# Optimization experiments

Measured on AMD Instinct MI355X. Metric: run time of the kernel, lower is better.

Reference implementation:

```python
import jax, jax.numpy as jnp
import numpy as np

LAYERS = 20
STACKS = 2
LPS = LAYERS // STACKS  # layers per stack -> dilations 2**(l % LPS)
OUT_CH = 256
RES_CH = 64
GATE_CH = 128
SKIP_CH = 256


def setup_inputs() -> dict:
    key = jax.random.key(0)
    ks = jax.random.split(key, 16)
    B, T = 8, 16000
    s = 0.05
    inp = {
        "x": jax.random.normal(ks[0], (B, OUT_CH, T), dtype=jnp.float32),
        # first causal conv (note: original code applies w_pre to the shifted
        # input twice -> output is 2*w_pre(pre); w_cur is unused, so omitted)
        "w_pre0": jax.random.normal(ks[1], (RES_CH, OUT_CH)) * s,
        "b_pre0": jax.random.normal(ks[2], (RES_CH,)) * s,
        # per-layer dilated conv (no bias), residual block, skip projection
        "w_dil_pre": jax.random.normal(ks[3], (LAYERS, GATE_CH, RES_CH)) * s,
        "w_dil_cur": jax.random.normal(ks[4], (LAYERS, GATE_CH, RES_CH)) * s,
        "bias_h": jax.random.normal(ks[5], (LAYERS, GATE_CH)) * s,
        "w_res": jax.random.normal(ks[6], (LAYERS, RES_CH, RES_CH)) * s,
        "b_res": jax.random.normal(ks[7], (LAYERS, RES_CH)) * s,
        "w_skip": jax.random.normal(ks[8], (LAYERS, SKIP_CH, RES_CH)) * s,
        "b_skip": jax.random.normal(ks[9], (LAYERS, SKIP_CH)) * s,
        # output head
        "w_relu": jax.random.normal(ks[10], (SKIP_CH, SKIP_CH)) * s,
        "b_relu": jax.random.normal(ks[11], (SKIP_CH,)) * s,
        "w_out": jax.random.normal(ks[12], (OUT_CH, SKIP_CH)) * s,
        "b_out": jax.random.normal(ks[13], (OUT_CH,)) * s,
    }
    return inp


def _shift_right(h, d):
    # causal shift: pad d zeros on the left along time, drop last d samples
    return jnp.pad(h, ((0, 0), (0, 0), (d, 0)))[:, :, :-d]


def reference(x, w_pre0, b_pre0, w_dil_pre, w_dil_cur, bias_h,
              w_res, b_res, w_skip, b_skip, w_relu, b_relu, w_out, b_out):
    # first causal conv: original Conv2X1 'casual' path computes
    # w_pre(pre) + w_pre(pre) = 2 * w_pre(pre)  (faithful to source)
    pre = _shift_right(x, 1)
    h = 2.0 * (jnp.einsum('rc,bct->brt', w_pre0, pre) + b_pre0[None, :, None])

    skip = jnp.zeros((x.shape[0], SKIP_CH, x.shape[2]), dtype=h.dtype)
    for l in range(LAYERS):
        d = 2 ** (l % LPS)
        h_pre = _shift_right(h, d)
        # dilated 2x1 conv = two channel-wise linears (no bias), summed with bias_h
        a = (jnp.einsum('gr,brt->bgt', w_dil_pre[l], h_pre)
             + jnp.einsum('gr,brt->bgt', w_dil_cur[l], h)
             + bias_h[l][None, :, None])
        g = jnp.tanh(a[:, :RES_CH]) * jax.nn.sigmoid(a[:, RES_CH:])
        res = jnp.einsum('rq,bqt->brt', w_res[l], g) + b_res[l][None, :, None]
        h = h + res
        skip = skip + jnp.einsum('sr,brt->bst', w_skip[l], g) + b_skip[l][None, :, None]

    o = jax.nn.relu(skip)
    o = jnp.einsum('ps,bst->bpt', w_relu, o) + b_relu[None, :, None]
    o = jax.nn.relu(o)
    logits = jnp.einsum('os,bst->bot', w_out, o) + b_out[None, :, None]
    return jax.nn.softmax(logits, axis=1)  # (B, out_channels, T)
```

## Files before the change

### kernel.cpp

```cpp
#include <hip/hip_runtime.h>
#include <math.h>

#define B_ 8
#define T_ 16000
#define NBT 250
#define HROWS 16512
#define NLAY 20

typedef __attribute__((ext_vector_type(8))) short bf16x8;
typedef __attribute__((ext_vector_type(4))) float f32x4;
typedef __attribute__((ext_vector_type(4))) short sh4;

__device__ __forceinline__ unsigned short f2bf(float f){
  unsigned u = __float_as_uint(f);
  u += 0x7fffu + ((u >> 16) & 1u);
  return (unsigned short)(u >> 16);
}
__device__ __forceinline__ float bf2f(unsigned short s){
  return __uint_as_float(((unsigned)s) << 16);
}
__device__ __forceinline__ void split2(float v, unsigned short& hi, unsigned short& lo){
  hi = f2bf(v);
  lo = f2bf(v - bf2f(hi));
}

#define MFMA(a,b,c) __builtin_amdgcn_mfma_f32_16x16x32_bf16((a),(b),(c),0,0,0)

__device__ __forceinline__ void gload16(const short* gsrc, short* ldst){
  __builtin_amdgcn_global_load_lds(
      (const __attribute__((address_space(1))) unsigned int*)gsrc,
      (__attribute__((address_space(3))) unsigned int*)ldst, 16, 0, 0);
}

__global__ void k_split(const float* __restrict__ src, short* __restrict__ hi,
                        short* __restrict__ lo, int n){
  int idx = blockIdx.x * 256 + threadIdx.x;
  if (idx < n){
    unsigned short h, l; split2(src[idx], h, l);
    hi[idx] = (short)h; lo[idx] = (short)l;
  }
}
__global__ void k_split_gate(const float* __restrict__ wdp, const float* __restrict__ wdc,
                             short* __restrict__ hi, short* __restrict__ lo){
  int idx = blockIdx.x * 256 + threadIdx.x;
  if (idx < NLAY*128*128){
    int l   = idx >> 14;
    int rem = idx & 16383;
    int row = rem >> 7;
    int k   = rem & 127;
    float v = (k < 64) ? wdp[(l*128 + row)*64 + k] : wdc[(l*128 + row)*64 + (k-64)];
    unsigned short h, lo16; split2(v, h, lo16);
    hi[idx] = (short)h; lo[idx] = (short)lo16;
  }
}
__global__ void k_pack_wsf(const float* __restrict__ wsk, short* __restrict__ wsf){
  int idx = blockIdx.x * 256 + threadIdx.x;
  if (idx < NLAY*8*2*2*64*8){
    int e    = idx & 7;
    int j    = (idx >> 3) & 63;
    int kb2  = (idx >> 9) & 1;
    int half = (idx >> 10) & 1;
    int w    = (idx >> 11) & 7;
    int l    = idx >> 14;
    int row  = w*32 + half*16 + (j & 15);
    int ch   = (kb2*4 + (j >> 4))*8 + e;
    wsf[idx] = (short)f2bf(wsk[((size_t)l*256 + row)*64 + ch]);
  }
}
__global__ void k_bsum(const float* __restrict__ bsk, float* __restrict__ bsum){
  int s = threadIdx.x;
  if (s < 256){
    float a = 0.f;
#pragma unroll
    for (int l = 0; l < NLAY; ++l) a += bsk[l*256 + s];
    bsum[s] = a;
  }
}
__global__ void k_zero_guard(short* __restrict__ hA, short* __restrict__ hB){
  int idx = blockIdx.x * 256 + threadIdx.x;
  if (idx < B_*512*128){
    int b = idx / (512*128);
    int rem = idx - b*(512*128);
    size_t off = (size_t)b*HROWS*128 + rem;
    hA[off] = 0; hB[off] = 0;
  }
}

__global__ __launch_bounds__(512) void k_head_in(
    const float* __restrict__ x, const short* __restrict__ wph,
    const short* __restrict__ wpl, const float* __restrict__ bias,
    short* __restrict__ h)
{
  __shared__ short SXh[64*256], SXl[64*256];
  const int tid = threadIdx.x;
  const int bb = blockIdx.x / NBT;
  const int t0 = (blockIdx.x % NBT) * 64;
  const int lane = tid & 63, w = tid >> 6;
  const int l16 = lane & 15, l4 = lane >> 4;

  const float* xb = x + (size_t)bb * 256 * T_;
  {
    int col = lane;
    int t = t0 + col - 1;
#pragma unroll
    for (int p = 0; p < 16; ++p){
      int k0 = w*32 + p*2;
      float v0 = (t >= 0) ? xb[(size_t)k0*T_ + t] : 0.f;
      float v1 = (t >= 0) ? xb[(size_t)(k0+1)*T_ + t] : 0.f;
      unsigned short h0,l0,h1,l1; split2(v0,h0,l0); split2(v1,h1,l1);
      int idx = col*256 + (k0 ^ ((col & 15) << 3));
      ((unsigned int*)SXh)[idx>>1] = (unsigned)h0 | ((unsigned)h1 << 16);
      ((unsigned int*)SXl)[idx>>1] = (unsigned)l0 | ((unsigned)l1 << 16);
    }
  }
  __syncthreads();

  const int mi = w & 3, nh = w >> 2;
  const int rowA = mi*16 + l16;
  const int rt0 = mi*16 + l4*4;
  bf16x8 Ah[8], Al[8];
#pragma unroll
  for (int kb = 0; kb < 8; ++kb){
    int ko = kb*32 + l4*8;
    Ah[kb] = *(const bf16x8*)(wph + (size_t)rowA*256 + ko);
    Al[kb] = *(const bf16x8*)(wpl + (size_t)rowA*256 + ko);
  }
  short* hb = h + ((size_t)bb*HROWS + 512)*128;
#pragma unroll
  for (int nt = 0; nt < 2; ++nt){
    int col = (nh*2 + nt)*16 + l16;
    f32x4 acc = {0.f,0.f,0.f,0.f};
#pragma unroll
    for (int kb = 0; kb < 8; ++kb){
      int ko = (kb*32 + l4*8) ^ (l16 << 3);
      bf16x8 bhv = *(const bf16x8*)&SXh[col*256 + ko];
      bf16x8 blv = *(const bf16x8*)&SXl[col*256 + ko];
      acc = MFMA(Ah[kb], bhv, acc);
      acc = MFMA(Ah[kb], blv, acc);
      acc = MFMA(Al[kb], bhv, acc);
    }
    int t = t0 + col;
    int key = t & 15;
    int c  = rt0 >> 3, sub = rt0 & 7;
    sh4 hv, lv;
#pragma unroll
    for (int r = 0; r < 4; ++r){
      float v = 2.f*(acc[r] + bias[rt0 + r]);
      unsigned short hh, ll; split2(v, hh, ll);
      hv[r] = (short)hh; lv[r] = (short)ll;
    }
    *(sh4*)&hb[(size_t)t*128 + ((c ^ key) << 3) + sub] = hv;
    *(sh4*)&hb[(size_t)t*128 + (((c + 8) ^ key) << 3) + sub] = lv;
  }
}

__global__ __launch_bounds__(512, 6) void k_layer6(
    const short* __restrict__ hin, short* __restrict__ hout,
    short* __restrict__ gout,
    const short* __restrict__ wgh, const short* __restrict__ wgl,
    const short* __restrict__ wrh, const short* __restrict__ wrlo,
    const float* __restrict__ bh, const float* __restrict__ br, int d)
{
  __shared__ short SH[64*128];
  __shared__ short SHP[64*128];
  const int tid = threadIdx.x;
  const int bb = blockIdx.x / NBT;
  const int tile = blockIdx.x % NBT;
  const int t0 = tile * 64;
  const int lane = tid & 63, w = tid >> 6;
  const int l16 = lane & 15, l4 = lane >> 4;

  const short* hb = hin + ((size_t)bb*HROWS + 512)*128;
  {
#pragma unroll
    for (int i = 0; i < 2; ++i){
      int colb = (w*2 + i)*4;
      const short* s1 = hb + (size_t)(t0 + colb + (lane>>4))*128 + (lane&15)*8;
      gload16(s1, &SH[colb*128]);
      const short* s2 = hb + (size_t)(t0 - d + colb + (lane>>4))*128 + (lane&15)*8;
      gload16(s2, &SHP[colb*128]);
    }
  }

  const int mi = w & 3, nh = w >> 2;
  const int rt0 = mi*16 + l4*4;
  const int rowt = mi*16 + l16, rows = 64 + mi*16 + l16;
  float bt[4], bs[4];
#pragma unroll
  for (int r = 0; r < 4; ++r){ bt[r] = bh[rt0+r]; bs[r] = bh[64+rt0+r]; }
  __syncthreads();

  f32x4 at0 = {0.f,0.f,0.f,0.f}, at1 = {0.f,0.f,0.f,0.f};
  f32x4 as0 = {0.f,0.f,0.f,0.f}, as1 = {0.f,0.f,0.f,0.f};
  {
#pragma unroll
    for (int kb = 0; kb < 2; ++kb){
      int ko = kb*32 + l4*8;
      bf16x8 Wth = *(const bf16x8*)(wgh + (size_t)rowt*128 + ko);
      bf16x8 Wtl = *(const bf16x8*)(wgl + (size_t)rowt*128 + ko);
      bf16x8 Wsh = *(const bf16x8*)(wgh + (size_t)rows*128 + ko);
      bf16x8 Wsl = *(const bf16x8*)(wgl + (size_t)rows*128 + ko);
      int cb = kb*4 + l4;
#pragma unroll
      for (int nt = 0; nt < 2; ++nt){
        int col = (nh*2 + nt)*16 + l16;
        int keyP = (col - d) & 15;
        bf16x8 bhv = *(const bf16x8*)&SHP[col*128 + ((cb ^ keyP) << 3)];
        bf16x8 blv = *(const bf16x8*)&SHP[col*128 + (((cb + 8) ^ keyP) << 3)];
        if (nt == 0){
          at0 = MFMA(Wth, bhv, at0); at0 = MFMA(Wth, blv, at0); at0 = MFMA(Wtl, bhv, at0);
          as0 = MFMA(Wsh, bhv, as0); as0 = MFMA(Wsh, blv, as0); as0 = MFMA(Wsl, bhv, as0);
        } else {
          at1 = MFMA(Wth, bhv, at1); at1 = MFMA(Wth, blv, at1); at1 = MFMA(Wtl, bhv, at1);
          as1 = MFMA(Wsh, bhv, as1); as1 = MFMA(Wsh, blv, as1); as1 = MFMA(Wsl, bhv, as1);
        }
      }
    }
  }
  {
#pragma unroll
    for (int kb = 2; kb < 4; ++kb){
      int ko = kb*32 + l4*8;
      bf16x8 Wth = *(const bf16x8*)(wgh + (size_t)rowt*128 + ko);
      bf16x8 Wtl = *(const bf16x8*)(wgl + (size_t)rowt*128 + ko);
      bf16x8 Wsh = *(const bf16x8*)(wgh + (size_t)rows*128 + ko);
      bf16x8 Wsl = *(const bf16x8*)(wgl + (size_t)rows*128 + ko);
      int cb = (kb & 1)*4 + l4;
#pragma unroll
      for (int nt = 0; nt < 2; ++nt){
        int col = (nh*2 + nt)*16 + l16;
        int keyC = col & 15;
        bf16x8 bhv = *(const bf16x8*)&SH[col*128 + ((cb ^ keyC) << 3)];
        bf16x8 blv = *(const bf16x8*)&SH[col*128 + (((cb + 8) ^ keyC) << 3)];
        if (nt == 0){
          at0 = MFMA(Wth, bhv, at0); at0 = MFMA(Wth, blv, at0); at0 = MFMA(Wtl, bhv, at0);
          as0 = MFMA(Wsh, bhv, as0); as0 = MFMA(Wsh, blv, as0); as0 = MFMA(Wsl, bhv, as0);
        } else {
          at1 = MFMA(Wth, bhv, at1); at1 = MFMA(Wth, blv, at1); at1 = MFMA(Wtl, bhv, at1);
          as1 = MFMA(Wsh, bhv, as1); as1 = MFMA(Wsh, blv, as1); as1 = MFMA(Wsl, bhv, as1);
        }
      }
    }
  }

  unsigned gp[2][4];
#pragma unroll
  for (int nt = 0; nt < 2; ++nt){
    unsigned short gh4[4], gl4[4];
#pragma unroll
    for (int r = 0; r < 4; ++r){
      float av = ((nt == 0) ? at0[r] : at1[r]) + bt[r];
      float sv = ((nt == 0) ? as0[r] : as1[r]) + bs[r];
      float e2 = __expf(2.f*av);
      float tv = 1.f - 2.f/(e2 + 1.f);
      float sg = 1.f/(1.f + __expf(-sv));
      float g  = tv*sg;
      split2(g, gh4[r], gl4[r]);
    }
    gp[nt][0] = (unsigned)gh4[0] | ((unsigned)gh4[1] << 16);
    gp[nt][1] = (unsigned)gh4[2] | ((unsigned)gh4[3] << 16);
    gp[nt][2] = (unsigned)gl4[0] | ((unsigned)gl4[1] << 16);
    gp[nt][3] = (unsigned)gl4[2] | ((unsigned)gl4[3] << 16);
  }
  __syncthreads();

  short* SGh = SHP;
  short* SGl = SHP + 4096;
#pragma unroll
  for (int nt = 0; nt < 2; ++nt){
    int col = (nh*2 + nt)*16 + l16;
    int gib = col*64 + (rt0 ^ ((col & 7) << 3));
    ((unsigned int*)&SGh[gib])[0] = gp[nt][0];
    ((unsigned int*)&SGh[gib])[1] = gp[nt][1];
    ((unsigned int*)&SGl[gib])[0] = gp[nt][2];
    ((unsigned int*)&SGl[gib])[1] = gp[nt][3];
  }
  __syncthreads();

  {
    int f = tid >> 6, j = tid & 63;
    int row = (f >> 1)*16 + (j & 15);
    int c   = (f & 1)*4 + (j >> 4);
    bf16x8 v = *(const bf16x8*)&SGh[row*64 + ((c ^ (row & 7)) << 3)];
    *(bf16x8*)(gout + ((size_t)bb*NBT + tile)*4096 + tid*8) = v;
  }

  {
    const int rowA = mi*16 + l16;
    bf16x8 Rh[2], Rl[2];
#pragma unroll
    for (int kb = 0; kb < 2; ++kb){
      int ko = kb*32 + l4*8;
      Rh[kb] = *(const bf16x8*)(wrh  + (size_t)rowA*64 + ko);
      Rl[kb] = *(const bf16x8*)(wrlo + (size_t)rowA*64 + ko);
    }
    short* ho = hout + ((size_t)bb*HROWS + 512)*128;
    const int cH = rt0 >> 3, sub = rt0 & 7;
#pragma unroll
    for (int nt = 0; nt < 2; ++nt){
      int col = (nh*2 + nt)*16 + l16;
      int keyC = col & 15;
      f32x4 acc = {0.f,0.f,0.f,0.f};
#pragma unroll
      for (int kb = 0; kb < 2; ++kb){
        int ko = (kb*32 + l4*8) ^ ((col & 7) << 3);
        bf16x8 bhv = *(const bf16x8*)&SGh[col*64 + ko];
        bf16x8 blv = *(const bf16x8*)&SGl[col*64 + ko];
        acc = MFMA(Rh[kb], bhv, acc);
        acc = MFMA(Rh[kb], blv, acc);
        acc = MFMA(Rl[kb], bhv, acc);
      }
      sh4 hi4 = *(const sh4*)&SH[col*128 + ((cH ^ keyC) << 3) + sub];
      sh4 lo4 = *(const sh4*)&SH[col*128 + (((cH + 8) ^ keyC) << 3) + sub];
      int t = t0 + col;
      sh4 hv, lv;
#pragma unroll
      for (int r = 0; r < 4; ++r){
        float hin_f = bf2f((unsigned short)hi4[r]) + bf2f((unsigned short)lo4[r]);
        float v = hin_f + acc[r] + br[rt0 + r];
        unsigned short hh, ll; split2(v, hh, ll);
        hv[r] = (short)hh; lv[r] = (short)ll;
      }
      *(sh4*)&ho[(size_t)t*128 + ((cH ^ keyC) << 3) + sub] = hv;
      *(sh4*)&ho[(size_t)t*128 + (((cH + 8) ^ keyC) << 3) + sub] = lv;
    }
  }
}

__global__ __launch_bounds__(512) void k_head_fused(
    float* __restrict__ io,
    const short* __restrict__ g,
    const short* __restrict__ wsf,
    const float* __restrict__ bsum,
    const short* __restrict__ wrlh, const short* __restrict__ wrll,
    const float* __restrict__ brl,
    const short* __restrict__ woh, const short* __restrict__ wol,
    const float* __restrict__ bo)
{
  __shared__ short S1h[64*256];
  const int tid = threadIdx.x;
  const int bb = blockIdx.x / NBT;
  const int tile = blockIdx.x % NBT;
  const int t0 = tile * 64;
  const int lane = tid & 63, w = tid >> 6;
  const int l16 = lane & 15, l4 = lane >> 4;

  const int r0 = w*32 + l16, r1 = w*32 + 16 + l16;
  const int rtb0 = w*32 + l4*4, rtb1 = rtb0 + 16;

  const int rh = w >> 2, ntw = w & 3;
  f32x4 acc[8];
#pragma unroll
  for (int m = 0; m < 8; ++m) acc[m] = (f32x4){0.f,0.f,0.f,0.f};
  {
    const size_t LSTR = (size_t)B_ * NBT * 4096;
    const short* gfrag = g + ((size_t)bb*NBT + tile)*4096 + (ntw*2)*512 + lane*8;
    const short* wbase = wsf + (size_t)rh*4*2048 + lane*8;
    for (int l20 = 0; l20 < 20; ++l20){
      bf16x8 B0 = *(const bf16x8*)(gfrag + (size_t)l20*LSTR);
      bf16x8 B1 = *(const bf16x8*)(gfrag + (size_t)l20*LSTR + 512);
      const short* wl = wbase + (size_t)l20*16384;
#pragma unroll
      for (int m = 0; m < 8; ++m){
        const short* wm = wl + (m >> 1)*2048 + (m & 1)*1024;
        bf16x8 A0 = *(const bf16x8*)(wm);
        bf16x8 A1 = *(const bf16x8*)(wm + 512);
        acc[m] = MFMA(A0, B0, acc[m]);
        acc[m] = MFMA(A1, B1, acc[m]);
      }
    }
  }

  {
    const int c2 = ntw*16 + l16;
#pragma unroll
    for (int m = 0; m < 8; ++m){
      int rtb = rh*128 + m*16 + l4*4;
      unsigned short h[4];
#pragma unroll
      for (int r = 0; r < 4; ++r)
        h[r] = f2bf(fmaxf(acc[m][r] + bsum[rtb + r], 0.f));
      int i0 = c2*256 + (rtb ^ (l16 << 3));
      ((unsigned int*)&S1h[i0])[0] = (unsigned)h[0] | ((unsigned)h[1] << 16);
      ((unsigned int*)&S1h[i0])[1] = (unsigned)h[2] | ((unsigned)h[3] << 16);
    }
  }
  __syncthreads();

  f32x4 acc0[4], acc1[4];
#pragma unroll
  for (int nt = 0; nt < 4; ++nt){ acc0[nt] = (f32x4){0.f,0.f,0.f,0.f}; acc1[nt] = (f32x4){0.f,0.f,0.f,0.f}; }
#pragma unroll
  for (int kb = 0; kb < 8; ++kb){
    int ko = kb*32 + l4*8;
    bf16x8 A0h = *(const bf16x8*)(wrlh + (size_t)r0*256 + ko);
    bf16x8 A0l = *(const bf16x8*)(wrll + (size_t)r0*256 + ko);
    bf16x8 A1h = *(const bf16x8*)(wrlh + (size_t)r1*256 + ko);
    bf16x8 A1l = *(const bf16x8*)(wrll + (size_t)r1*256 + ko);
#pragma unroll
    for (int nt = 0; nt < 4; ++nt){
      int c2 = nt*16 + l16;
      int kos = ko ^ (l16 << 3);
      bf16x8 bhv = *(const bf16x8*)&S1h[c2*256 + kos];
      acc0[nt] = MFMA(A0h, bhv, acc0[nt]);
      acc0[nt] = MFMA(A0l, bhv, acc0[nt]);
      acc1[nt] = MFMA(A1h, bhv, acc1[nt]);
      acc1[nt] = MFMA(A1l, bhv, acc1[nt]);
    }
  }
  __syncthreads();
  {
    float br0[4], br1[4];
#pragma unroll
    for (int r = 0; r < 4; ++r){ br0[r] = brl[rtb0+r]; br1[r] = brl[rtb1+r]; }
#pragma unroll
    for (int nt = 0; nt < 4; ++nt){
      int c2 = nt*16 + l16;
      unsigned short h[4];
#pragma unroll
      for (int r = 0; r < 4; ++r)
        h[r] = f2bf(fmaxf(acc0[nt][r] + br0[r], 0.f));
      int i0 = c2*256 + (rtb0 ^ (l16 << 3));
      ((unsigned int*)&S1h[i0])[0] = (unsigned)h[0] | ((unsigned)h[1] << 16);
      ((unsigned int*)&S1h[i0])[1] = (unsigned)h[2] | ((unsigned)h[3] << 16);
#pragma unroll
      for (int r = 0; r < 4; ++r)
        h[r] = f2bf(fmaxf(acc1[nt][r] + br1[r], 0.f));
      int i1 = c2*256 + (rtb1 ^ (l16 << 3));
      ((unsigned int*)&S1h[i1])[0] = (unsigned)h[0] | ((unsigned)h[1] << 16);
      ((unsigned int*)&S1h[i1])[1] = (unsigned)h[2] | ((unsigned)h[3] << 16);
    }
  }
  __syncthreads();

#pragma unroll
  for (int nt = 0; nt < 4; ++nt){ acc0[nt] = (f32x4){0.f,0.f,0.f,0.f}; acc1[nt] = (f32x4){0.f,0.f,0.f,0.f}; }
#pragma unroll
  for (int kb = 0; kb < 8; ++kb){
    int ko = kb*32 + l4*8;
    bf16x8 A0h = *(const bf16x8*)(woh + (size_t)r0*256 + ko);
    bf16x8 A0l = *(const bf16x8*)(wol + (size_t)r0*256 + ko);
    bf16x8 A1h = *(const bf16x8*)(woh + (size_t)r1*256 + ko);
    bf16x8 A1l = *(const bf16x8*)(wol + (size_t)r1*256 + ko);
#pragma unroll
    for (int nt = 0; nt < 4; ++nt){
      int c2 = nt*16 + l16;
      int kos = ko ^ (l16 << 3);
      bf16x8 bhv = *(const bf16x8*)&S1h[c2*256 + kos];
      acc0[nt] = MFMA(A0h, bhv, acc0[nt]);
      acc0[nt] = MFMA(A0l, bhv, acc0[nt]);
      acc1[nt] = MFMA(A1h, bhv, acc1[nt]);
      acc1[nt] = MFMA(A1l, bhv, acc1[nt]);
    }
  }
  __syncthreads();
  float* smax = (float*)S1h;
  float* ssum = smax + 512;
  float* iob = io + (size_t)bb * 256 * T_;
  float bo0[4], bo1[4];
#pragma unroll
  for (int r = 0; r < 4; ++r){ bo0[r] = bo[rtb0+r]; bo1[r] = bo[rtb1+r]; }
#pragma unroll
  for (int nt = 0; nt < 4; ++nt){
    float m = -1e30f;
#pragma unroll
    for (int r = 0; r < 4; ++r){
      acc0[nt][r] += bo0[r];
      acc1[nt][r] += bo1[r];
      m = fmaxf(m, fmaxf(acc0[nt][r], acc1[nt][r]));
    }
    m = fmaxf(m, __shfl_xor(m, 16, 64));
    m = fmaxf(m, __shfl_xor(m, 32, 64));
    smax[w*64 + nt*16 + l16] = m;
  }
  __syncthreads();
#pragma unroll
  for (int nt = 0; nt < 4; ++nt){
    float m = smax[nt*16 + l16];
#pragma unroll
    for (int ww = 1; ww < 8; ++ww) m = fmaxf(m, smax[ww*64 + nt*16 + l16]);
    float s = 0.f;
#pragma unroll
    for (int r = 0; r < 4; ++r){
      acc0[nt][r] = __expf(acc0[nt][r] - m); s += acc0[nt][r];
      acc1[nt][r] = __expf(acc1[nt][r] - m); s += acc1[nt][r];
    }
    s += __shfl_xor(s, 16, 64);
    s += __shfl_xor(s, 32, 64);
    ssum[w*64 + nt*16 + l16] = s;
  }
  __syncthreads();
#pragma unroll
  for (int nt = 0; nt < 4; ++nt){
    float S = 0.f;
#pragma unroll
    for (int ww = 0; ww < 8; ++ww) S += ssum[ww*64 + nt*16 + l16];
    float inv = 1.f / S;
    int t = t0 + nt*16 + l16;
#pragma unroll
    for (int r = 0; r < 4; ++r){
      iob[(size_t)(rtb0 + r)*T_ + t] = acc0[nt][r]*inv;
      iob[(size_t)(rtb1 + r)*T_ + t] = acc1[nt][r]*inv;
    }
  }
}

extern "C" void kernel_launch(void* const* d_in, const int* in_sizes, int n_in,
                              void* d_out, int out_size, void* d_ws, size_t ws_size,
                              hipStream_t stream) {
  const float* x       = (const float*)d_in[0];
  const float* w_pre0  = (const float*)d_in[1];
  const float* b_pre0  = (const float*)d_in[2];
  const float* w_dil_p = (const float*)d_in[3];
  const float* w_dil_c = (const float*)d_in[4];
  const float* bias_h  = (const float*)d_in[5];
  const float* w_res   = (const float*)d_in[6];
  const float* b_res   = (const float*)d_in[7];
  const float* w_skip  = (const float*)d_in[8];
  const float* b_skip  = (const float*)d_in[9];
  const float* w_relu  = (const float*)d_in[10];
  const float* b_relu  = (const float*)d_in[11];
  const float* w_out   = (const float*)d_in[12];
  const float* b_out   = (const float*)d_in[13];

  float* out = (float*)d_out;
  short* hA = (short*)d_ws;
  short* hB = hA + (size_t)B_ * HROWS * 128;
  float* bsum = (float*)(hB + (size_t)B_ * HROWS * 128);
  short* p   = (short*)(bsum + 256);
  short* WPh = p; p += 16384;  short* WPl = p; p += 16384;
  short* WGh = p; p += 327680; short* WGl = p; p += 327680;
  short* WRh = p; p += 81920;  short* WRl = p; p += 81920;
  short* WSF = p; p += 327680;
  short* WLh = p; p += 65536;  short* WLl = p; p += 65536;
  short* WOh = p; p += 65536;  short* WOl = p; p += 65536;
  short* GBUF = p;

  k_split<<<64, 256, 0, stream>>>(w_pre0, WPh, WPl, 16384);
  k_split_gate<<<1280, 256, 0, stream>>>(w_dil_p, w_dil_c, WGh, WGl);
  k_split<<<320, 256, 0, stream>>>(w_res, WRh, WRl, 81920);
  k_pack_wsf<<<1280, 256, 0, stream>>>(w_skip, WSF);
  k_split<<<256, 256, 0, stream>>>(w_relu, WLh, WLl, 65536);
  k_split<<<256, 256, 0, stream>>>(w_out, WOh, WOl, 65536);
  k_zero_guard<<<2048, 256, 0, stream>>>(hA, hB);
  k_bsum<<<1, 256, 0, stream>>>(b_skip, bsum);

  k_head_in<<<B_ * NBT, 512, 0, stream>>>(x, WPh, WPl, b_pre0, hA);

  const short* hin = hA;
  short* houtp = hB;
  for (int l = 0; l < NLAY; ++l) {
    int d = 1 << (l % 10);
    k_layer6<<<B_ * NBT, 512, 0, stream>>>(
        hin, houtp,
        GBUF + (size_t)l * B_ * NBT * 4096,
        WGh + (size_t)l*16384, WGl + (size_t)l*16384,
        WRh + (size_t)l*4096,  WRl + (size_t)l*4096,
        bias_h + (size_t)l*128, b_res + (size_t)l*64, d);
    const short* tmp = hin;
    hin = houtp;
    houtp = (short*)tmp;
  }

  k_head_fused<<<B_ * NBT, 512, 0, stream>>>(
      out, GBUF, WSF, bsum, WLh, WLl, b_relu, WOh, WOl, b_out);
}
```

Before: 1.494 ms.

## Double-buffer skip-head gate fragments via global_load_lds with MFMA priority

In the fused head kernel's skip-accumulation loop, the per-layer gate fragments are now fetched asynchronously into a per-wave double-buffered LDS region with global_load_lds, prefetching layer l+1 while layer l is consumed. Weight fragments for a layer are loaded into registers up front, and the MFMA block is wrapped in sched barriers with raised wave priority. The aim is to hide global load latency behind the MFMA work. The cost is more registers for the unrolled A fragments and hand-written waitcnt sequencing, which is fragile if the compiler emits other vector memory ops in between.

```diff
diff --git a/kernel.cpp b/kernel.cpp
--- a/kernel.cpp
+++ b/kernel.cpp
@@ -30,6 +30,9 @@
   __builtin_amdgcn_global_load_lds(
       (const __attribute__((address_space(1))) unsigned int*)gsrc,
       (__attribute__((address_space(3))) unsigned int*)ldst, 16, 0, 0);
+}
+__device__ __forceinline__ unsigned ldsaddr(const short* p){
+  return (unsigned)(size_t)(const __attribute__((address_space(3))) short*)p;
 }
 
 __global__ void k_split(const float* __restrict__ src, short* __restrict__ hi,
@@ -337,7 +340,7 @@
     const short* __restrict__ woh, const short* __restrict__ wol,
     const float* __restrict__ bo)
 {
-  __shared__ short S1h[64*256];
+  __shared__ short POOL[16384];
   const int tid = threadIdx.x;
   const int bb = blockIdx.x / NBT;
   const int tile = blockIdx.x % NBT;
@@ -356,21 +359,49 @@
     const size_t LSTR = (size_t)B_ * NBT * 4096;
     const short* gfrag = g + ((size_t)bb*NBT + tile)*4096 + (ntw*2)*512 + lane*8;
     const short* wbase = wsf + (size_t)rh*4*2048 + lane*8;
+    short* myB = &POOL[w*2048];
+    const unsigned ba = ldsaddr(myB) + (unsigned)(lane * 16);
+
+#define STAGE2(l20, buf) do{ \
+      gload16(gfrag + (size_t)(l20)*LSTR,        &myB[(buf)*1024]); \
+      gload16(gfrag + (size_t)(l20)*LSTR + 512,  &myB[(buf)*1024 + 512]); }while(0)
+
+    STAGE2(0, 0);
     for (int l20 = 0; l20 < 20; ++l20){
-      bf16x8 B0 = *(const bf16x8*)(gfrag + (size_t)l20*LSTR);
-      bf16x8 B1 = *(const bf16x8*)(gfrag + (size_t)l20*LSTR + 512);
       const short* wl = wbase + (size_t)l20*16384;
+      bf16x8 A[8][2];
 #pragma unroll
       for (int m = 0; m < 8; ++m){
         const short* wm = wl + (m >> 1)*2048 + (m & 1)*1024;
-        bf16x8 A0 = *(const bf16x8*)(wm);
-        bf16x8 A1 = *(const bf16x8*)(wm + 512);
-        acc[m] = MFMA(A0, B0, acc[m]);
-        acc[m] = MFMA(A1, B1, acc[m]);
-      }
-    }
-  }
-
+        A[m][0] = *(const bf16x8*)(wm);
+        A[m][1] = *(const bf16x8*)(wm + 512);
+      }
+      if (l20 + 1 < 20){
+        STAGE2(l20 + 1, (l20 + 1) & 1);
+        asm volatile("s_waitcnt vmcnt(2)" ::: "memory");
+      } else {
+        asm volatile("s_waitcnt vmcnt(0)" ::: "memory");
+      }
+      bf16x8 B0, B1;
+      unsigned a0 = ba + (unsigned)((l20 & 1) * 2048);
+      asm volatile("ds_read_b128 %0, %1" : "=&v"(B0) : "v"(a0) : "memory");
+      asm volatile("ds_read_b128 %0, %1 offset:1024" : "=&v"(B1) : "v"(a0) : "memory");
+      asm volatile("s_waitcnt lgkmcnt(0)" ::: "memory");
+      __builtin_amdgcn_sched_barrier(0);
+      __builtin_amdgcn_s_setprio(1);
+#pragma unroll
+      for (int m = 0; m < 8; ++m){
+        acc[m] = MFMA(A[m][0], B0, acc[m]);
+        acc[m] = MFMA(A[m][1], B1, acc[m]);
+      }
+      __builtin_amdgcn_s_setprio(0);
+      __builtin_amdgcn_sched_barrier(0);
+    }
+#undef STAGE2
+  }
+  __syncthreads();
+
+  short* S1h = POOL;
   {
     const int c2 = ntw*16 + l16;
 #pragma unroll
@@ -454,7 +485,7 @@
     }
   }
   __syncthreads();
-  float* smax = (float*)S1h;
+  float* smax = (float*)POOL;
   float* ssum = smax + 512;
   float* iob = io + (size_t)bb * 256 * T_;
   float bo0[4], bo1[4];
```

Result: no change. 1.482 ms (-0.8%).
